# Kernel optimization log

Hardware: AMD Instinct MI355X
Metric: run time of the kernel (lower is better)

The kernel has to match this reference:

```python
import jax, jax.numpy as jnp
import numpy as np

N = 100000   # vertices
T = 128      # temporal depth
E = 1600000  # edges (avg degree 16)
K = 9        # conv kernel size
PAD = 4      # 'same' padding -> T preserved
L = 3        # number of layers


def setup_inputs() -> dict:
    key = jax.random.key(0)
    ks = jax.random.split(key, 6)
    x = jax.random.normal(ks[0], (N, T), dtype=jnp.float32)
    edge_index = jax.random.randint(ks[1], (2, E), 0, N, dtype=jnp.int32)
    conv_w = jax.random.normal(ks[2], (L, 1, 1, K), dtype=jnp.float32) * (1.0 / np.sqrt(K))
    conv_b = jax.random.normal(ks[3], (L, 1), dtype=jnp.float32) * 0.1
    W_out = jax.random.normal(ks[4], (3, N), dtype=jnp.float32) * (1.0 / np.sqrt(N))
    b_out = jax.random.normal(ks[5], (3,), dtype=jnp.float32) * 0.1
    return {"x": x, "edge_index": edge_index, "conv_w": conv_w,
            "conv_b": conv_b, "W_out": W_out, "b_out": b_out}


def _conv1d(x, w, b):
    # x: [N, T], w: [1, 1, K] (OIH), b: [1]; torch Conv1d = cross-correlation.
    y = jax.lax.conv_general_dilated(
        x[:, None, :], w, window_strides=(1,), padding=[(PAD, PAD)],
        dimension_numbers=("NCH", "OIH", "NCH"))
    return y[:, 0, :] + b  # [N, T]


def reference(x, edge_index, conv_w, conv_b, W_out, b_out):
    # add_self_loops: append (i, i) for every node
    loop = jnp.arange(N, dtype=edge_index.dtype)
    src = jnp.concatenate([edge_index[0], loop])  # message sources
    dst = jnp.concatenate([edge_index[1], loop])  # aggregation targets
    # in-degree counts (>=1 due to self loops) for mean aggregation
    cnt = jax.ops.segment_sum(jnp.ones(src.shape, jnp.float32), dst,
                              num_segments=N)[:, None]  # [N, 1]
    for i in range(L):
        h = _conv1d(x, conv_w[i], conv_b[i])                    # [N, T]
        s = jax.ops.segment_sum(h[src], dst, num_segments=N)    # scatter-sum of gathered msgs
        x = jax.nn.relu(s / cnt)                                # mean aggr + relu
    x = x.reshape(-1, N)            # [T, N] (row-major view like torch .view)
    return x @ W_out.T + b_out      # [T, 3]
```

## Files before the change

kernel.cpp:

```cpp
#include <hip/hip_runtime.h>

#define NN 100000
#define TT 128
#define EE 1600000
#define KK 9

#define BSH 9
#define BMASK 511
#define NBUCK 196
#define BCAP 10240
#define EPB 4096
#define BINB 391
#define CVTB 3125

#define OSLICE 1568
#define ONS 64
#define OTG 16

typedef _Float16 f16;
typedef __attribute__((ext_vector_type(2))) _Float16 f16x2;
typedef __attribute__((ext_vector_type(4))) _Float16 f16x4;
typedef __attribute__((ext_vector_type(8))) _Float16 f16x8;

union HU8 { f16x8 h; int4 i; };

__global__ __launch_bounds__(1024)
void bin_cvt_kernel(const int* __restrict__ ei, int* __restrict__ gcursor,
                    unsigned int* __restrict__ binned,
                    const float4* __restrict__ x, f16x4* __restrict__ x16) {
    __shared__ int hist[NBUCK];
    __shared__ int gbase[NBUCK];
    int tid = threadIdx.x;

    if (blockIdx.x >= BINB) {
        int i = (blockIdx.x - BINB) * 1024 + tid;
        float4 v = x[i];
        f16x4 o;
        o.x = (f16)v.x; o.y = (f16)v.y; o.z = (f16)v.z; o.w = (f16)v.w;
        x16[i] = o;
        return;
    }

    if (tid < NBUCK) hist[tid] = 0;
    __syncthreads();
    int base = blockIdx.x * EPB;
    unsigned int val[4];
    short bkt[4];
    short rank[4];
#pragma unroll
    for (int k = 0; k < 4; k++) {
        int e = base + k * 1024 + tid;
        bkt[k] = -1;
        if (e < EE) {
            int s = ei[e];
            int d = ei[EE + e];
            bkt[k] = (short)(d >> BSH);
            val[k] = ((unsigned int)(d & BMASK) << 20) | (unsigned int)s;
            rank[k] = (short)atomicAdd(&hist[bkt[k]], 1);
        }
    }
    __syncthreads();
    if (tid < NBUCK) gbase[tid] = hist[tid] ? atomicAdd(&gcursor[tid], hist[tid]) : 0;
    __syncthreads();
#pragma unroll
    for (int k = 0; k < 4; k++) {
        if (bkt[k] >= 0)
            binned[(size_t)bkt[k] * BCAP + gbase[bkt[k]] + (int)rank[k]] = val[k];
    }
}

__global__ __launch_bounds__(1024)
void bucket_csr_kernel(const unsigned int* __restrict__ binned,
                       const int* __restrict__ gcursor,
                       int* __restrict__ offsets,
                       float* __restrict__ inv_cnt,
                       int* __restrict__ col) {
    __shared__ int hist[512];
    __shared__ int cur[512];
    __shared__ int smB[256];
    __shared__ int sc[512];
    int b = blockIdx.x;
    int tid = threadIdx.x;

    if (tid < 256) smB[tid] = (tid < NBUCK) ? gcursor[tid] : 0;
    __syncthreads();
    for (int off = 1; off < 256; off <<= 1) {
        int v = 0;
        if (tid < 256 && tid >= off) v = smB[tid - off];
        __syncthreads();
        if (tid < 256) smB[tid] += v;
        __syncthreads();
    }
    int bucket_base = (b == 0) ? 0 : smB[b - 1];
    if (b == 0 && tid == 0) offsets[NN] = EE;

    int cnt = gcursor[b];
    const unsigned int* ePtr = binned + (size_t)b * BCAP;
    if (tid < 512) hist[tid] = 0;
    __syncthreads();
    for (int j = tid; j < cnt; j += 1024)
        atomicAdd(&hist[ePtr[j] >> 20], 1);
    __syncthreads();
    int d = (tid < 512) ? hist[tid] : 0;
    if (tid < 512) sc[tid] = d;
    __syncthreads();
    for (int off = 1; off < 512; off <<= 1) {
        int v = 0;
        if (tid < 512 && tid >= off) v = sc[tid - off];
        __syncthreads();
        if (tid < 512) sc[tid] += v;
        __syncthreads();
    }
    if (tid < 512) {
        int node = (b << BSH) + tid;
        int pos = bucket_base + sc[tid] - d;
        if (node < NN) {
            offsets[node] = pos;
            inv_cnt[node] = 1.0f / (1.0f + (float)d);
            cur[tid] = pos;
        }
    }
    __syncthreads();
    for (int j = tid; j < cnt; j += 1024) {
        unsigned int v = ePtr[j];
        int pos = atomicAdd(&cur[v >> 20], 1);
        col[pos] = (int)(v & 0xFFFFF);
    }
}

__device__ __forceinline__ void gather_conv_node(
    const f16x8* __restrict__ xin, const int* __restrict__ offsets,
    const int* __restrict__ col, const float* __restrict__ inv_cnt,
    const float* wr, float bb, int node, int lane, int q, int p, float* s)
{
    int lo = offsets[node], hi = offsets[node + 1];
    int cnt = hi - lo;
    int my_col = (lane < cnt) ? col[lo + lane] : 0;
    int jn = cnt < 64 ? cnt : 64;

    const f16 z = (f16)0;
    f16x8 acc0 = {z, z, z, z, z, z, z, z};
    f16x8 acc1 = {z, z, z, z, z, z, z, z};

    int j = 0;
    for (; j + 7 < jn; j += 8) {
        int c0 = __shfl(my_col, j + q);
        int c1 = __shfl(my_col, j + 4 + q);
        f16x8 v0 = xin[(c0 << 4) | p];
        f16x8 v1 = xin[(c1 << 4) | p];
        acc0 += v0;
        acc1 += v1;
    }
    for (; j + 3 < jn; j += 4) {
        int c = __shfl(my_col, j + q);
        acc0 += xin[(c << 4) | p];
    }
    if (j < jn) {
        int rem = jn - j;
        int c = __shfl(my_col, j + (q < rem ? q : 0));
        f16x8 v = xin[(c << 4) | p];
        if (q < rem) acc1 += v;
    }
    for (int k = 64; k < cnt; k++) {
        int c = col[lo + k];
        f16x8 v = xin[(c << 4) | p];
        if (q == 0) acc0 += v;
    }
    acc0 += acc1;

    {
        HU8 u; u.h = acc0;
        int4 o;
        o.x = __shfl_xor(u.i.x, 16); o.y = __shfl_xor(u.i.y, 16);
        o.z = __shfl_xor(u.i.z, 16); o.w = __shfl_xor(u.i.w, 16);
        HU8 w2; w2.i = o;
        acc0 += w2.h;
        u.h = acc0;
        o.x = __shfl_xor(u.i.x, 32); o.y = __shfl_xor(u.i.y, 32);
        o.z = __shfl_xor(u.i.z, 32); o.w = __shfl_xor(u.i.w, 32);
        w2.i = o;
        acc0 += w2.h;
    }

    f16x8 sv = xin[(node << 4) | p];
    float A[16];
    A[4]  = (float)acc0[0] + (float)sv[0];
    A[5]  = (float)acc0[1] + (float)sv[1];
    A[6]  = (float)acc0[2] + (float)sv[2];
    A[7]  = (float)acc0[3] + (float)sv[3];
    A[8]  = (float)acc0[4] + (float)sv[4];
    A[9]  = (float)acc0[5] + (float)sv[5];
    A[10] = (float)acc0[6] + (float)sv[6];
    A[11] = (float)acc0[7] + (float)sv[7];
#pragma unroll
    for (int i = 0; i < 4; i++) {
        A[i]      = __shfl_up(A[8 + i], 1, 16);
        A[12 + i] = __shfl_down(A[4 + i], 1, 16);
    }
    if (p == 0)  { A[0] = 0.0f; A[1] = 0.0f; A[2] = 0.0f; A[3] = 0.0f; }
    if (p == 15) { A[12] = 0.0f; A[13] = 0.0f; A[14] = 0.0f; A[15] = 0.0f; }

    float ic = inv_cnt[node];
#pragma unroll
    for (int i = 0; i < 8; i++) {
        float t = 0.0f;
#pragma unroll
        for (int k = 0; k < KK; k++) t += wr[k] * A[i + k];
        s[i] = fmaxf(t * ic + bb, 0.0f);
    }
}

__global__ __launch_bounds__(1024)
void fused_layer_kernel(const f16x8* __restrict__ xin,
                        const int* __restrict__ offsets,
                        const int* __restrict__ col,
                        const float* __restrict__ inv_cnt,
                        const float* __restrict__ w9,
                        const float* __restrict__ bptr,
                        f16x8* __restrict__ yout) {
    int tid = threadIdx.x;
    int lane = tid & 63;
    int q = lane >> 4;
    int p = lane & 15;
    int node = blockIdx.x * 16 + (tid >> 6);
    float wr[KK];
#pragma unroll
    for (int k = 0; k < KK; k++) wr[k] = w9[k];
    float s[8];
    gather_conv_node(xin, offsets, col, inv_cnt, wr, bptr[0], node, lane, q, p, s);
    if (q == 0) {
        f16x8 o;
#pragma unroll
        for (int i = 0; i < 8; i++) o[i] = (f16)s[i];
        yout[(node << 4) | p] = o;
    }
}

__global__ void out_partial_kernel(const f16* __restrict__ y3,
                                   const float* __restrict__ Wout,
                                   float* __restrict__ partial) {
    __shared__ float red[4][3];
    int sp = blockIdx.x;
    int tg = blockIdx.y;
    int tid = threadIdx.x;
    int lane = tid & 63;
    int wave = tid >> 6;
    int n0 = sp * OSLICE;
    int n1 = n0 + OSLICE;
    if (n1 > NN) n1 = NN;
    for (int t = tg * 8; t < tg * 8 + 8; t++) {
        const f16* yrow = y3 + (size_t)t * NN;
        float a0 = 0.0f, a1 = 0.0f, a2 = 0.0f;
        for (int n = n0 + tid * 2; n < n1; n += 512) {
            f16x2 v = *(const f16x2*)(yrow + n);
            float vx = (float)v.x, vy = (float)v.y;
            float2 wA = *(const float2*)(Wout + n);
            float2 wB = *(const float2*)(Wout + NN + n);
            float2 wC = *(const float2*)(Wout + 2 * NN + n);
            a0 += vx * wA.x + vy * wA.y;
            a1 += vx * wB.x + vy * wB.y;
            a2 += vx * wC.x + vy * wC.y;
        }
        for (int o = 32; o > 0; o >>= 1) {
            a0 += __shfl_down(a0, o);
            a1 += __shfl_down(a1, o);
            a2 += __shfl_down(a2, o);
        }
        if (lane == 0) {
            red[wave][0] = a0;
            red[wave][1] = a1;
            red[wave][2] = a2;
        }
        __syncthreads();
        if (tid == 0) {
            int idx = (t * ONS + sp) * 3;
            partial[idx + 0] = red[0][0] + red[1][0] + red[2][0] + red[3][0];
            partial[idx + 1] = red[0][1] + red[1][1] + red[2][1] + red[3][1];
            partial[idx + 2] = red[0][2] + red[1][2] + red[2][2] + red[3][2];
        }
        __syncthreads();
    }
}

__global__ void out_reduce_kernel(const float* __restrict__ partial,
                                  const float* __restrict__ bout,
                                  float* __restrict__ out) {
    int t = blockIdx.x;
    int l = threadIdx.x;
    int idx = (t * ONS + l) * 3;
    float a0 = partial[idx + 0];
    float a1 = partial[idx + 1];
    float a2 = partial[idx + 2];
    for (int o = 32; o > 0; o >>= 1) {
        a0 += __shfl_down(a0, o);
        a1 += __shfl_down(a1, o);
        a2 += __shfl_down(a2, o);
    }
    if (l == 0) {
        out[t * 3 + 0] = bout[0] + a0;
        out[t * 3 + 1] = bout[1] + a1;
        out[t * 3 + 2] = bout[2] + a2;
    }
}

extern "C" void kernel_launch(void* const* d_in, const int* in_sizes, int n_in,
                              void* d_out, int out_size, void* d_ws, size_t ws_size,
                              hipStream_t stream) {
    const float4* x    = (const float4*)d_in[0];
    const int*    ei   = (const int*)d_in[1];
    const float*  cw   = (const float*)d_in[2];
    const float*  cb   = (const float*)d_in[3];
    const float*  Wout = (const float*)d_in[4];
    const float*  bout = (const float*)d_in[5];
    float* out = (float*)d_out;

    char* ws = (char*)d_ws;
    size_t off = 0;
    auto alloc = [&](size_t bytes) -> void* {
        void* p = ws + off;
        off += (bytes + 255) & ~(size_t)255;
        return p;
    };
    f16x8*        x16     = (f16x8*)alloc((size_t)NN * TT * 2);
    f16x8*        yA      = (f16x8*)alloc((size_t)NN * TT * 2);
    f16x8*        yB      = (f16x8*)alloc((size_t)NN * TT * 2);
    unsigned int* binned  = (unsigned int*)alloc((size_t)NBUCK * BCAP * 4);
    int*          gcursor = (int*)alloc((size_t)NBUCK * 4);
    int*          offsets = (int*)alloc((size_t)(NN + 1) * 4);
    float*        inv_cnt = (float*)alloc((size_t)NN * 4);
    int*          col     = (int*)alloc((size_t)EE * 4);
    float*        partial = (float*)alloc((size_t)TT * ONS * 3 * 4);

    hipMemsetAsync(gcursor, 0, (size_t)NBUCK * 4, stream);
    bin_cvt_kernel<<<BINB + CVTB, 1024, 0, stream>>>(ei, gcursor, binned, x, (f16x4*)x16);
    bucket_csr_kernel<<<NBUCK, 1024, 0, stream>>>(binned, gcursor, offsets, inv_cnt, col);

    fused_layer_kernel<<<NN / 16, 1024, 0, stream>>>(x16, offsets, col, inv_cnt,
                                                     cw + 0 * KK, cb + 0, yA);
    fused_layer_kernel<<<NN / 16, 1024, 0, stream>>>(yA, offsets, col, inv_cnt,
                                                     cw + 1 * KK, cb + 1, yB);
    fused_layer_kernel<<<NN / 16, 1024, 0, stream>>>(yB, offsets, col, inv_cnt,
                                                     cw + 2 * KK, cb + 2, yA);

    out_partial_kernel<<<dim3(ONS, OTG), 256, 0, stream>>>((const f16*)yA, Wout, partial);
    out_reduce_kernel<<<TT, 64, 0, stream>>>(partial, bout, out);
}
```

Before: 352.5 us.

## Shrink layer blocks to 256 threads and fold output reduction into last block

The fused layer kernel now runs 4 nodes per 256-thread block instead of 16 nodes per 1024-thread block, and its launch bounds are dropped. Smaller blocks should reduce tail imbalance from variable-degree nodes and give the compiler more register freedom. Separately, the final reduce kernel is removed: out_partial blocks bump an atomic counter, and the last block to finish sums the partials and adds the bias. This saves a kernel launch but adds a threadfence and atomic to every block, and the final sum runs serially over 64 slices per thread.

Measured after the change: 400.8 us. 13.7% more time.

```diff
diff --git a/kernel.cpp b/kernel.cpp
--- a/kernel.cpp
+++ b/kernel.cpp
@@ -210,19 +210,18 @@
     }
 }
 
-__global__ __launch_bounds__(1024)
-void fused_layer_kernel(const f16x8* __restrict__ xin,
-                        const int* __restrict__ offsets,
-                        const int* __restrict__ col,
-                        const float* __restrict__ inv_cnt,
-                        const float* __restrict__ w9,
-                        const float* __restrict__ bptr,
-                        f16x8* __restrict__ yout) {
+__global__ void fused_layer_kernel(const f16x8* __restrict__ xin,
+                                   const int* __restrict__ offsets,
+                                   const int* __restrict__ col,
+                                   const float* __restrict__ inv_cnt,
+                                   const float* __restrict__ w9,
+                                   const float* __restrict__ bptr,
+                                   f16x8* __restrict__ yout) {
     int tid = threadIdx.x;
     int lane = tid & 63;
     int q = lane >> 4;
     int p = lane & 15;
-    int node = blockIdx.x * 16 + (tid >> 6);
+    int node = blockIdx.x * 4 + (tid >> 6);
     float wr[KK];
 #pragma unroll
     for (int k = 0; k < KK; k++) wr[k] = w9[k];
@@ -238,8 +237,12 @@
 
 __global__ void out_partial_kernel(const f16* __restrict__ y3,
                                    const float* __restrict__ Wout,
-                                   float* __restrict__ partial) {
+                                   float* __restrict__ partial,
+                                   int* __restrict__ counter,
+                                   const float* __restrict__ bout,
+                                   float* __restrict__ out) {
     __shared__ float red[4][3];
+    __shared__ int is_last;
     int sp = blockIdx.x;
     int tg = blockIdx.y;
     int tid = threadIdx.x;
@@ -280,23 +283,25 @@
         }
         __syncthreads();
     }
-}
-
-__global__ void out_reduce_kernel(const float* __restrict__ partial,
-                                  const float* __restrict__ bout,
-                                  float* __restrict__ out) {
-    int t = blockIdx.x;
-    int l = threadIdx.x;
-    int idx = (t * ONS + l) * 3;
-    float a0 = partial[idx + 0];
-    float a1 = partial[idx + 1];
-    float a2 = partial[idx + 2];
-    for (int o = 32; o > 0; o >>= 1) {
-        a0 += __shfl_down(a0, o);
-        a1 += __shfl_down(a1, o);
-        a2 += __shfl_down(a2, o);
-    }
-    if (l == 0) {
+
+    __threadfence();
+    if (tid == 0) {
+        int prev = atomicAdd(counter, 1);
+        is_last = (prev == ONS * OTG - 1);
+    }
+    __syncthreads();
+    if (!is_last) return;
+    __threadfence();
+    if (tid < TT) {
+        int t = tid;
+        float a0 = 0.0f, a1 = 0.0f, a2 = 0.0f;
+        const float* pr = partial + (size_t)t * ONS * 3;
+#pragma unroll 4
+        for (int s2 = 0; s2 < ONS; s2++) {
+            a0 += pr[s2 * 3 + 0];
+            a1 += pr[s2 * 3 + 1];
+            a2 += pr[s2 * 3 + 2];
+        }
         out[t * 3 + 0] = bout[0] + a0;
         out[t * 3 + 1] = bout[1] + a1;
         out[t * 3 + 2] = bout[2] + a2;
@@ -324,24 +329,25 @@
     f16x8*        x16     = (f16x8*)alloc((size_t)NN * TT * 2);
     f16x8*        yA      = (f16x8*)alloc((size_t)NN * TT * 2);
     f16x8*        yB      = (f16x8*)alloc((size_t)NN * TT * 2);
+    int*          gcursor = (int*)alloc((size_t)(NBUCK + 64) * 4);
     unsigned int* binned  = (unsigned int*)alloc((size_t)NBUCK * BCAP * 4);
-    int*          gcursor = (int*)alloc((size_t)NBUCK * 4);
     int*          offsets = (int*)alloc((size_t)(NN + 1) * 4);
     float*        inv_cnt = (float*)alloc((size_t)NN * 4);
     int*          col     = (int*)alloc((size_t)EE * 4);
     float*        partial = (float*)alloc((size_t)TT * ONS * 3 * 4);
-
-    hipMemsetAsync(gcursor, 0, (size_t)NBUCK * 4, stream);
+    int*          counter = gcursor + NBUCK;
+
+    hipMemsetAsync(gcursor, 0, (size_t)(NBUCK + 1) * 4, stream);
     bin_cvt_kernel<<<BINB + CVTB, 1024, 0, stream>>>(ei, gcursor, binned, x, (f16x4*)x16);
     bucket_csr_kernel<<<NBUCK, 1024, 0, stream>>>(binned, gcursor, offsets, inv_cnt, col);
 
-    fused_layer_kernel<<<NN / 16, 1024, 0, stream>>>(x16, offsets, col, inv_cnt,
-                                                     cw + 0 * KK, cb + 0, yA);
-    fused_layer_kernel<<<NN / 16, 1024, 0, stream>>>(yA, offsets, col, inv_cnt,
-                                                     cw + 1 * KK, cb + 1, yB);
-    fused_layer_kernel<<<NN / 16, 1024, 0, stream>>>(yB, offsets, col, inv_cnt,
-                                                     cw + 2 * KK, cb + 2, yA);
-
-    out_partial_kernel<<<dim3(ONS, OTG), 256, 0, stream>>>((const f16*)yA, Wout, partial);
-    out_reduce_kernel<<<TT, 64, 0, stream>>>(partial, bout, out);
-}
+    fused_layer_kernel<<<NN / 4, 256, 0, stream>>>(x16, offsets, col, inv_cnt,
+                                                   cw + 0 * KK, cb + 0, yA);
+    fused_layer_kernel<<<NN / 4, 256, 0, stream>>>(yA, offsets, col, inv_cnt,
+                                                   cw + 1 * KK, cb + 1, yB);
+    fused_layer_kernel<<<NN / 4, 256, 0, stream>>>(yB, offsets, col, inv_cnt,
+                                                   cw + 2 * KK, cb + 2, yA);
+
+    out_partial_kernel<<<dim3(ONS, OTG), 256, 0, stream>>>((const f16*)yA, Wout, partial,
+                                                           counter, bout, out);
+}
```
